# Kernel tuning notes

Measured on AMD Instinct MI355X. Metric: run time of the kernel, lower is better.

Reference implementation:

```python
import jax, jax.numpy as jnp
import numpy as np

D_HEAD = 64      # per-head dim (init d_head)
WINDOW = 64      # sliding_window_size
ROPE_BASE = 10000.0


def _rope(x):
    # x: [B, H, L, d] ; standard half-split rotary embedding over positions 0..L-1
    L, d = x.shape[-2], x.shape[-1]
    half = d // 2
    inv_freq = 1.0 / (ROPE_BASE ** (jnp.arange(half, dtype=jnp.float32) / half))
    ang = jnp.arange(L, dtype=jnp.float32)[:, None] * inv_freq  # [L, half]
    cos, sin = jnp.cos(ang), jnp.sin(ang)
    x1, x2 = x[..., :half], x[..., half:]
    return jnp.concatenate([x1 * cos - x2 * sin, x1 * sin + x2 * cos], axis=-1)


def setup_inputs() -> dict:
    key = jax.random.key(0)
    ks = jax.random.split(key, 4)
    B, L, D, H = 4, 2048, 2048, 2048
    nh = H // D_HEAD
    S = 16  # num_sinks
    u = jax.random.normal(ks[0], (B, L, D), jnp.float32)
    Wqkv = jax.random.normal(ks[1], (3 * H, D), jnp.float32) / np.sqrt(D)
    bqkv = jnp.zeros((3 * H,), jnp.float32)
    Wo = jax.random.normal(ks[2], (D, H), jnp.float32) / np.sqrt(H)
    bo = jnp.zeros((D,), jnp.float32)
    sinks = jax.random.normal(ks[3], (nh, S, D_HEAD), jnp.float32) / np.sqrt(D_HEAD)
    return {"u": u, "Wqkv": Wqkv, "bqkv": bqkv, "Wo": Wo, "bo": bo, "sinks": sinks}


def reference(u, Wqkv, bqkv, Wo, bo, sinks):
    B, L, D = u.shape
    d, w = D_HEAD, WINDOW
    nh, S, _ = sinks.shape
    scale = 1.0 / np.sqrt(d)

    qkv = u @ Wqkv.T + bqkv                         # [B, L, 3H]
    q, k, v = jnp.split(qkv, 3, axis=-1)
    heads = lambda x: x.reshape(B, L, nh, d).transpose(0, 2, 1, 3)  # [B, nh, L, d]
    q, k, v = heads(q), heads(k), heads(v)
    q, k = _rope(q), _rope(k)

    # Banded (sliding-window) attention in blocks of size w: query block i
    # attends key blocks {i-1, i, i+1} plus S global sink tokens.
    # Sink queries (prepended in the original) are discarded by O[:, :, -L:],
    # so we only compute attention for the L real queries.
    nb = L // w
    Qb = q.reshape(B, nh, nb, w, d)
    Kb = k.reshape(B, nh, nb, w, d)
    Vb = v.reshape(B, nh, nb, w, d)

    blk = jnp.arange(nb)[:, None] + jnp.arange(-1, 2)[None, :]   # [nb, 3]
    valid = (blk >= 0) & (blk < nb)
    blkc = jnp.clip(blk, 0, nb - 1)
    Kband = Kb[:, :, blkc].reshape(B, nh, nb, 3 * w, d)
    Vband = Vb[:, :, blkc].reshape(B, nh, nb, 3 * w, d)

    qpos = (jnp.arange(nb) * w)[:, None] + jnp.arange(w)          # [nb, w]
    kpos = ((blkc * w)[..., None] + jnp.arange(w)).reshape(nb, 3 * w)
    vmask = jnp.broadcast_to(valid[:, :, None], (nb, 3, w)).reshape(nb, 3 * w)
    mask = vmask[:, None, :] & (jnp.abs(qpos[:, :, None] - kpos[:, None, :]) <= w)  # [nb, w, 3w]

    s_band = jnp.einsum('bhnqd,bhnkd->bhnqk', Qb, Kband) * scale
    s_band = jnp.where(mask, s_band, -jnp.inf)
    s_sink = jnp.einsum('bhnqd,hsd->bhnqs', Qb, sinks) * scale    # sink K = sink param (no RoPE)
    p = jax.nn.softmax(jnp.concatenate([s_sink, s_band], axis=-1), axis=-1)

    O = (jnp.einsum('bhnqs,hsd->bhnqd', p[..., :S], sinks)        # sink V = sink param
         + jnp.einsum('bhnqk,bhnkd->bhnqd', p[..., S:], Vband))
    y = O.reshape(B, nh, L, d).transpose(0, 2, 1, 3).reshape(B, L, nh * d)
    return y @ Wo.T + bo
```

## Files before the change

### kernel.cpp

```cpp
#include <hip/hip_runtime.h>
#include <hip/hip_bf16.h>

typedef unsigned short u16;
typedef __attribute__((ext_vector_type(8))) short bf16x8;
typedef __attribute__((ext_vector_type(4))) float f32x4;

__device__ __forceinline__ u16 f2b(float f) {
  union { __hip_bfloat16 h; u16 u; } cv;
  cv.h = __float2bfloat16(f);
  return cv.u;
}
__device__ __forceinline__ float b2f(u16 u) {
  union { unsigned int i; float f; } cv;
  cv.i = ((unsigned int)u) << 16;
  return cv.f;
}

__global__ void cvt_bf16(const float* __restrict__ in, u16* __restrict__ out) {
  size_t i = ((size_t)blockIdx.x * 256 + threadIdx.x) * 4;
  float4 v = *(const float4*)(in + i);
  ushort4 o;
  o.x = f2b(v.x); o.y = f2b(v.y); o.z = f2b(v.z); o.w = f2b(v.w);
  *(ushort4*)(out + i) = o;
}

__global__ void rope_tab_k(float2* __restrict__ tab) {
  int t = blockIdx.x * 256 + threadIdx.x;
  int l = t >> 5, i = t & 31;
  float inv = powf(10000.0f, -(float)i * (1.0f / 32.0f));
  float ang = (float)l * inv;
  tab[t] = make_float2(cosf(ang), sinf(ang));
}

__global__ void rope_apply_k(u16* __restrict__ qkv, const float2* __restrict__ tab) {
  int idx = blockIdx.x * 256 + threadIdx.x;
  int i = idx & 31, h = (idx >> 5) & 31, row = idx >> 10;
  int l = row & 2047;
  float2 cs = tab[(l << 5) + i];
  size_t base = (size_t)row * 6144 + h * 64;
  #pragma unroll
  for (int t = 0; t < 2; ++t) {
    float x1 = b2f(qkv[base + i]);
    float x2 = b2f(qkv[base + 32 + i]);
    qkv[base + i]      = f2b(x1 * cs.x - x2 * cs.y);
    qkv[base + 32 + i] = f2b(x1 * cs.y + x2 * cs.x);
    base += 2048;
  }
}

template<bool BF16OUT>
__global__ __launch_bounds__(256) void gemm_bt(const u16* __restrict__ A,
                                               const u16* __restrict__ Bm,
                                               const float* __restrict__ bias,
                                               u16* __restrict__ Cb,
                                               float* __restrict__ Cf,
                                               int Ncols) {
  __shared__ u16 As[128 * 32];
  __shared__ u16 Bs[128 * 32];
  const int tid = threadIdx.x;
  const int lane = tid & 63, wid = tid >> 6;
  const int wr = wid >> 1, wc = wid & 1;
  const int m0 = blockIdx.y * 128, n0 = blockIdx.x * 128;
  const int lrow = lane >> 2;
  const int lcb  = (lane & 3) * 16;
  const int fr = lane & 15;
  const int fkb = (lane >> 4) * 16;
  f32x4 acc[4][4] = {};
  for (int k0 = 0; k0 < 2048; k0 += 32) {
    #pragma unroll
    for (int j = 0; j < 2; ++j) {
      int chunk = wid * 2 + j;
      int row = chunk * 16 + lrow;
      const char* ga = (const char*)(A + (size_t)(m0 + row) * 2048 + k0) + lcb;
      const char* gb = (const char*)(Bm + (size_t)(n0 + row) * 2048 + k0) + lcb;
      __builtin_amdgcn_global_load_lds((const __attribute__((address_space(1))) unsigned int*)ga,
                                       (__attribute__((address_space(3))) unsigned int*)(As + chunk * 512),
                                       16, 0, 0);
      __builtin_amdgcn_global_load_lds((const __attribute__((address_space(1))) unsigned int*)gb,
                                       (__attribute__((address_space(3))) unsigned int*)(Bs + chunk * 512),
                                       16, 0, 0);
    }
    __syncthreads();
    bf16x8 af[4], bfr[4];
    #pragma unroll
    for (int m = 0; m < 4; ++m)
      af[m] = *(const bf16x8*)((const char*)As + (wr * 64 + m * 16 + fr) * 64 + fkb);
    #pragma unroll
    for (int n = 0; n < 4; ++n)
      bfr[n] = *(const bf16x8*)((const char*)Bs + (wc * 64 + n * 16 + fr) * 64 + fkb);
    #pragma unroll
    for (int m = 0; m < 4; ++m)
      #pragma unroll
      for (int n = 0; n < 4; ++n)
        acc[m][n] = __builtin_amdgcn_mfma_f32_16x16x32_bf16(af[m], bfr[n], acc[m][n], 0, 0, 0);
    __syncthreads();
  }
  #pragma unroll
  for (int m = 0; m < 4; ++m) {
    #pragma unroll
    for (int n = 0; n < 4; ++n) {
      int gcol = n0 + wc * 64 + n * 16 + fr;
      int grow0 = m0 + wr * 64 + m * 16 + (lane >> 4) * 4;
      float bv = bias[gcol];
      #pragma unroll
      for (int r = 0; r < 4; ++r) {
        float v = acc[m][n][r] + bv;
        if (BF16OUT) Cb[(size_t)(grow0 + r) * Ncols + gcol] = f2b(v);
        else         Cf[(size_t)(grow0 + r) * Ncols + gcol] = v;
      }
    }
  }
}

#define PSTR 232
__global__ __launch_bounds__(256) void attn_k(const u16* __restrict__ qkv,
                                              const float* __restrict__ sinks,
                                              u16* __restrict__ O) {
  __shared__ char smem[59392];
  char* Kraw = smem;
  char* Qraw = smem + 28672;
  u16* Ps = (u16*)smem;
  u16* Vt = (u16*)(smem + 29696);
  const int tid = threadIdx.x, lane = tid & 63, wid = tid >> 6;
  const int fr = lane & 15, fk = lane >> 4;
  const int bx = blockIdx.x;
  const int n = bx & 31, h = (bx >> 5) & 31, b = bx >> 10;
  const size_t qrow0 = (size_t)b * 2048 + n * 64;

  for (int c = tid; c < 512; c += 256) {
    int row = c >> 3, colb = (c & 7) * 16;
    uint4 v = *(const uint4*)((const char*)(qkv + (qrow0 + row) * 6144 + h * 64) + colb);
    *(uint4*)(Qraw + ((row * 128 + colb) ^ ((row & 7) << 4))) = v;
  }
  {
    int row = tid >> 4, col4 = (tid & 15) * 4;
    float4 v = *(const float4*)(sinks + ((size_t)h * 16 + row) * 64 + col4);
    ushort4 o; o.x = f2b(v.x); o.y = f2b(v.y); o.z = f2b(v.z); o.w = f2b(v.w);
    *(ushort4*)(Kraw + ((row * 128 + col4 * 2) ^ ((row & 7) << 4))) = o;
  }
  for (int c = tid; c < 1536; c += 256) {
    int kidx = c >> 3, colb = (c & 7) * 16;
    int blk = n - 1 + (kidx >> 6);
    int blkc = min(max(blk, 0), 31);
    int kpos = blkc * 64 + (kidx & 63);
    uint4 v = *(const uint4*)((const char*)(qkv + ((size_t)b * 2048 + kpos) * 6144 + 2048 + h * 64) + colb);
    int row = 16 + kidx;
    *(uint4*)(Kraw + ((row * 128 + colb) ^ ((row & 7) << 4))) = v;
  }
  if (tid < 128) {
    int row = 208 + (tid >> 3), colb = (tid & 7) * 16;
    uint4 z = {0, 0, 0, 0};
    *(uint4*)(Kraw + ((row * 128 + colb) ^ ((row & 7) << 4))) = z;
  }
  __syncthreads();

  bf16x8 qf[2];
  {
    int qrow = wid * 16 + fr;
    #pragma unroll
    for (int kc = 0; kc < 2; ++kc)
      qf[kc] = *(const bf16x8*)(Qraw + ((qrow * 128 + kc * 64 + fk * 16) ^ ((qrow & 7) << 4)));
  }
  f32x4 sacc[14];
  #pragma unroll
  for (int g = 0; g < 14; ++g) {
    int key = g * 16 + fr;
    bf16x8 kf0 = *(const bf16x8*)(Kraw + ((key * 128 + fk * 16) ^ ((key & 7) << 4)));
    bf16x8 kf1 = *(const bf16x8*)(Kraw + ((key * 128 + 64 + fk * 16) ^ ((key & 7) << 4)));
    f32x4 a = {};
    a = __builtin_amdgcn_mfma_f32_16x16x32_bf16(qf[0], kf0, a, 0, 0, 0);
    a = __builtin_amdgcn_mfma_f32_16x16x32_bf16(qf[1], kf1, a, 0, 0, 0);
    sacc[g] = a;
  }
  float rowmax[4] = {-3e38f, -3e38f, -3e38f, -3e38f};
  #pragma unroll
  for (int g = 0; g < 14; ++g) {
    int key = g * 16 + fr;
    #pragma unroll
    for (int r = 0; r < 4; ++r) {
      float s = sacc[g][r] * 0.125f;
      bool valid;
      if (key < 16) valid = true;
      else if (key < 208) {
        int kidx = key - 16;
        int blk = n - 1 + (kidx >> 6);
        int kpos = blk * 64 + (kidx & 63);
        int qpos = n * 64 + wid * 16 + fk * 4 + r;
        valid = (blk >= 0) && (blk < 32) && (qpos - kpos <= 64) && (kpos - qpos <= 64);
      } else valid = false;
      s = valid ? s : -1e30f;
      sacc[g][r] = s;
      rowmax[r] = fmaxf(rowmax[r], s);
    }
  }
  #pragma unroll
  for (int d = 1; d < 16; d <<= 1)
    #pragma unroll
    for (int r = 0; r < 4; ++r)
      rowmax[r] = fmaxf(rowmax[r], __shfl_xor(rowmax[r], d));
  float rowsum[4] = {0, 0, 0, 0};
  #pragma unroll
  for (int g = 0; g < 14; ++g)
    #pragma unroll
    for (int r = 0; r < 4; ++r) {
      float p = __expf(sacc[g][r] - rowmax[r]);
      sacc[g][r] = p;
      rowsum[r] += p;
    }
  #pragma unroll
  for (int d = 1; d < 16; d <<= 1)
    #pragma unroll
    for (int r = 0; r < 4; ++r)
      rowsum[r] += __shfl_xor(rowsum[r], d);
  __syncthreads();

  #pragma unroll
  for (int g = 0; g < 14; ++g)
    #pragma unroll
    for (int r = 0; r < 4; ++r)
      Ps[(wid * 16 + fk * 4 + r) * PSTR + g * 16 + fr] = f2b(sacc[g][r]);
  {
    int dout = tid & 63, kb = tid >> 6;
    #pragma unroll
    for (int key = kb; key < 16; key += 4)
      Vt[dout * PSTR + key] = f2b(sinks[((size_t)h * 16 + key) * 64 + dout]);
    for (int kidx = kb; kidx < 192; kidx += 4) {
      int blk = n - 1 + (kidx >> 6);
      int blkc = min(max(blk, 0), 31);
      int kpos = blkc * 64 + (kidx & 63);
      Vt[dout * PSTR + 16 + kidx] = qkv[((size_t)b * 2048 + kpos) * 6144 + 4096 + h * 64 + dout];
    }
    #pragma unroll
    for (int key = 208 + kb; key < 224; key += 4)
      Vt[dout * PSTR + key] = 0;
  }
  __syncthreads();

  f32x4 oacc[4] = {};
  #pragma unroll
  for (int kc = 0; kc < 7; ++kc) {
    bf16x8 pf = *(const bf16x8*)(Ps + (wid * 16 + fr) * PSTR + kc * 32 + fk * 8);
    #pragma unroll
    for (int gd = 0; gd < 4; ++gd) {
      bf16x8 vf = *(const bf16x8*)(Vt + (gd * 16 + fr) * PSTR + kc * 32 + fk * 8);
      oacc[gd] = __builtin_amdgcn_mfma_f32_16x16x32_bf16(pf, vf, oacc[gd], 0, 0, 0);
    }
  }
  #pragma unroll
  for (int gd = 0; gd < 4; ++gd)
    #pragma unroll
    for (int r = 0; r < 4; ++r) {
      int qrl = wid * 16 + fk * 4 + r;
      float v = oacc[gd][r] / rowsum[r];
      O[(qrow0 + qrl) * 2048 + h * 64 + gd * 16 + fr] = f2b(v);
    }
}

extern "C" void kernel_launch(void* const* d_in, const int* in_sizes, int n_in,
                              void* d_out, int out_size, void* d_ws, size_t ws_size,
                              hipStream_t stream) {
  const float* u     = (const float*)d_in[0];
  const float* Wqkv  = (const float*)d_in[1];
  const float* bqkv  = (const float*)d_in[2];
  const float* Wo    = (const float*)d_in[3];
  const float* bo    = (const float*)d_in[4];
  const float* sinks = (const float*)d_in[5];
  float* out = (float*)d_out;

  char* ws = (char*)d_ws;
  u16* u_bf   = (u16*)ws;
  u16* w1_bf  = (u16*)(ws + 33554432);
  u16* qkv_bf = (u16*)(ws + 58720256);
  float2* tab = (float2*)(ws + 159383552);
  u16* O_bf  = u_bf;
  u16* w2_bf = w1_bf;

  cvt_bf16<<<16384, 256, 0, stream>>>(u, u_bf);
  cvt_bf16<<<12288, 256, 0, stream>>>(Wqkv, w1_bf);
  rope_tab_k<<<256, 256, 0, stream>>>(tab);
  gemm_bt<true><<<dim3(48, 64), 256, 0, stream>>>(u_bf, w1_bf, bqkv, qkv_bf, nullptr, 6144);
  rope_apply_k<<<32768, 256, 0, stream>>>(qkv_bf, tab);
  attn_k<<<4096, 256, 0, stream>>>(qkv_bf, sinks, O_bf);
  cvt_bf16<<<4096, 256, 0, stream>>>(Wo, w2_bf);
  gemm_bt<false><<<dim3(16, 64), 256, 0, stream>>>(O_bf, w2_bf, bo, nullptr, out, 2048);
}
```

Measured before the change: 624.5 us.

## Replace GEMM with 256x256 multi-stage pipelined kernel and fuse RoPE into epilogue

Swaps the simple single-buffered 128x128 GEMM for a 256x256-tile, 512-thread kernel. It uses a 4-slot LDS ring with three stages of global-to-LDS prefetch, explicit vmcnt waits, an XOR-swizzled LDS layout to reduce bank conflicts, and setprio around the MFMA block. The RoPE rotation is folded into the QKV GEMM epilogue by pairing accumulator columns n and n^2, which removes the separate read-modify-write pass over qkv. In exchange it needs 128KB of dynamic LDS per block. The output GEMM launches only 256 blocks, which may underfill the GPU.

```diff
diff --git a/kernel.cpp b/kernel.cpp
--- a/kernel.cpp
+++ b/kernel.cpp
@@ -32,81 +32,107 @@
   tab[t] = make_float2(cosf(ang), sinf(ang));
 }
 
-__global__ void rope_apply_k(u16* __restrict__ qkv, const float2* __restrict__ tab) {
-  int idx = blockIdx.x * 256 + threadIdx.x;
-  int i = idx & 31, h = (idx >> 5) & 31, row = idx >> 10;
-  int l = row & 2047;
-  float2 cs = tab[(l << 5) + i];
-  size_t base = (size_t)row * 6144 + h * 64;
-  #pragma unroll
-  for (int t = 0; t < 2; ++t) {
-    float x1 = b2f(qkv[base + i]);
-    float x2 = b2f(qkv[base + 32 + i]);
-    qkv[base + i]      = f2b(x1 * cs.x - x2 * cs.y);
-    qkv[base + 32 + i] = f2b(x1 * cs.y + x2 * cs.x);
-    base += 2048;
-  }
-}
-
-template<bool BF16OUT>
-__global__ __launch_bounds__(256) void gemm_bt(const u16* __restrict__ A,
-                                               const u16* __restrict__ Bm,
-                                               const float* __restrict__ bias,
-                                               u16* __restrict__ Cb,
-                                               float* __restrict__ Cf,
-                                               int Ncols) {
-  __shared__ u16 As[128 * 32];
-  __shared__ u16 Bs[128 * 32];
-  const int tid = threadIdx.x;
-  const int lane = tid & 63, wid = tid >> 6;
-  const int wr = wid >> 1, wc = wid & 1;
-  const int m0 = blockIdx.y * 128, n0 = blockIdx.x * 128;
-  const int lrow = lane >> 2;
-  const int lcb  = (lane & 3) * 16;
-  const int fr = lane & 15;
-  const int fkb = (lane >> 4) * 16;
-  f32x4 acc[4][4] = {};
-  for (int k0 = 0; k0 < 2048; k0 += 32) {
-    #pragma unroll
-    for (int j = 0; j < 2; ++j) {
-      int chunk = wid * 2 + j;
-      int row = chunk * 16 + lrow;
-      const char* ga = (const char*)(A + (size_t)(m0 + row) * 2048 + k0) + lcb;
-      const char* gb = (const char*)(Bm + (size_t)(n0 + row) * 2048 + k0) + lcb;
-      __builtin_amdgcn_global_load_lds((const __attribute__((address_space(1))) unsigned int*)ga,
-                                       (__attribute__((address_space(3))) unsigned int*)(As + chunk * 512),
-                                       16, 0, 0);
-      __builtin_amdgcn_global_load_lds((const __attribute__((address_space(1))) unsigned int*)gb,
-                                       (__attribute__((address_space(3))) unsigned int*)(Bs + chunk * 512),
-                                       16, 0, 0);
-    }
-    __syncthreads();
-    bf16x8 af[4], bfr[4];
-    #pragma unroll
-    for (int m = 0; m < 4; ++m)
-      af[m] = *(const bf16x8*)((const char*)As + (wr * 64 + m * 16 + fr) * 64 + fkb);
+template<int NCOLS, bool ROPE>
+__global__ __launch_bounds__(512, 2) void gemm_p(const u16* __restrict__ A,
+                                                 const u16* __restrict__ Bm,
+                                                 const float* __restrict__ bias,
+                                                 u16* __restrict__ Cb,
+                                                 float* __restrict__ Cf,
+                                                 const float2* __restrict__ tab) {
+  extern __shared__ char smem[];
+  u16* Asl = (u16*)smem;
+  u16* Bsl = (u16*)(smem + 65536);
+  const int tid = threadIdx.x, lane = tid & 63, w = tid >> 6;
+  const int wr = w >> 2, wcn = w & 3;
+  const int fr = lane & 15, fk = lane >> 4;
+  const int m0 = blockIdx.y * 256, n0 = blockIdx.x * 256;
+  const int srow = lane >> 2;
+  const int gslot = (lane & 3) ^ ((lane >> 3) & 3);
+  const int c0 = w * 2, c1 = c0 + 1;
+  const int sel = (fr >> 1) & 3;
+  const int ka = (fk ^ sel) << 4;
+  f32x4 acc[8][4] = {};
+
+  auto stage = [&](int jj) {
+    int slot = jj & 3;
+    int kk = jj * 32 + gslot * 8;
+    u16* Ad = Asl + slot * 8192;
+    u16* Bd = Bsl + slot * 8192;
+    const u16* gA0 = A  + (size_t)(m0 + c0 * 16 + srow) * 2048 + kk;
+    const u16* gA1 = A  + (size_t)(m0 + c1 * 16 + srow) * 2048 + kk;
+    const u16* gB0 = Bm + (size_t)(n0 + c0 * 16 + srow) * 2048 + kk;
+    const u16* gB1 = Bm + (size_t)(n0 + c1 * 16 + srow) * 2048 + kk;
+    __builtin_amdgcn_global_load_lds((const __attribute__((address_space(1))) unsigned int*)gA0,
+        (__attribute__((address_space(3))) unsigned int*)(Ad + c0 * 512), 16, 0, 0);
+    __builtin_amdgcn_global_load_lds((const __attribute__((address_space(1))) unsigned int*)gA1,
+        (__attribute__((address_space(3))) unsigned int*)(Ad + c1 * 512), 16, 0, 0);
+    __builtin_amdgcn_global_load_lds((const __attribute__((address_space(1))) unsigned int*)gB0,
+        (__attribute__((address_space(3))) unsigned int*)(Bd + c0 * 512), 16, 0, 0);
+    __builtin_amdgcn_global_load_lds((const __attribute__((address_space(1))) unsigned int*)gB1,
+        (__attribute__((address_space(3))) unsigned int*)(Bd + c1 * 512), 16, 0, 0);
+  };
+
+  stage(0); stage(1); stage(2);
+  asm volatile("s_waitcnt vmcnt(8)" ::: "memory");
+  asm volatile("s_barrier" ::: "memory");
+
+  for (int j = 0; j < 64; ++j) {
+    if (j < 61) stage(j + 3);
+    const char* Ab = (const char*)(Asl + (j & 3) * 8192);
+    const char* Bb = (const char*)(Bsl + (j & 3) * 8192);
+    bf16x8 af[8], bv[4];
+    #pragma unroll
+    for (int m = 0; m < 8; ++m)
+      af[m] = *(const bf16x8*)(Ab + (wr * 128 + m * 16 + fr) * 64 + ka);
     #pragma unroll
     for (int n = 0; n < 4; ++n)
-      bfr[n] = *(const bf16x8*)((const char*)Bs + (wc * 64 + n * 16 + fr) * 64 + fkb);
-    #pragma unroll
-    for (int m = 0; m < 4; ++m)
+      bv[n] = *(const bf16x8*)(Bb + (wcn * 64 + n * 16 + fr) * 64 + ka);
+    __builtin_amdgcn_s_setprio(1);
+    #pragma unroll
+    for (int m = 0; m < 8; ++m)
       #pragma unroll
       for (int n = 0; n < 4; ++n)
-        acc[m][n] = __builtin_amdgcn_mfma_f32_16x16x32_bf16(af[m], bfr[n], acc[m][n], 0, 0, 0);
-    __syncthreads();
-  }
-  #pragma unroll
-  for (int m = 0; m < 4; ++m) {
+        acc[m][n] = __builtin_amdgcn_mfma_f32_16x16x32_bf16(af[m], bv[n], acc[m][n], 0, 0, 0);
+    __builtin_amdgcn_s_setprio(0);
+    if (j < 61)       asm volatile("s_waitcnt vmcnt(8)" ::: "memory");
+    else if (j == 61) asm volatile("s_waitcnt vmcnt(4)" ::: "memory");
+    else if (j == 62) asm volatile("s_waitcnt vmcnt(0)" ::: "memory");
+    asm volatile("s_waitcnt lgkmcnt(0)" ::: "memory");
+    asm volatile("s_barrier" ::: "memory");
+  }
+
+  #pragma unroll
+  for (int m = 0; m < 8; ++m) {
+    int grow0 = m0 + wr * 128 + m * 16 + fk * 4;
     #pragma unroll
     for (int n = 0; n < 4; ++n) {
-      int gcol = n0 + wc * 64 + n * 16 + fr;
-      int grow0 = m0 + wr * 64 + m * 16 + (lane >> 4) * 4;
-      float bv = bias[gcol];
-      #pragma unroll
-      for (int r = 0; r < 4; ++r) {
-        float v = acc[m][n][r] + bv;
-        if (BF16OUT) Cb[(size_t)(grow0 + r) * Ncols + gcol] = f2b(v);
-        else         Cf[(size_t)(grow0 + r) * Ncols + gcol] = v;
+      int gcol = n0 + wcn * 64 + n * 16 + fr;
+      if (ROPE) {
+        if (gcol < 4096) {
+          int c = gcol & 63;
+          int i = c & 31;
+          bool lo = c < 32;
+          float bx = bias[gcol], bp = bias[gcol ^ 32];
+          #pragma unroll
+          for (int r = 0; r < 4; ++r) {
+            int t = grow0 + r;
+            float2 cs = tab[((t & 2047) << 5) + i];
+            float xb = acc[m][n][r] + bx;
+            float pb = acc[m][n ^ 2][r] + bp;
+            float o = lo ? (xb * cs.x - pb * cs.y) : (pb * cs.y + xb * cs.x);
+            Cb[(size_t)t * NCOLS + gcol] = f2b(o);
+          }
+        } else {
+          float bx = bias[gcol];
+          #pragma unroll
+          for (int r = 0; r < 4; ++r)
+            Cb[(size_t)(grow0 + r) * NCOLS + gcol] = f2b(acc[m][n][r] + bx);
+        }
+      } else {
+        float bx = bias[gcol];
+        #pragma unroll
+        for (int r = 0; r < 4; ++r)
+          Cf[(size_t)(grow0 + r) * NCOLS + gcol] = acc[m][n][r] + bx;
       }
     }
   }
@@ -275,12 +301,16 @@
   u16* O_bf  = u_bf;
   u16* w2_bf = w1_bf;
 
+  hipFuncSetAttribute((const void*)gemm_p<6144, true>,
+                      hipFuncAttributeMaxDynamicSharedMemorySize, 131072);
+  hipFuncSetAttribute((const void*)gemm_p<2048, false>,
+                      hipFuncAttributeMaxDynamicSharedMemorySize, 131072);
+
   cvt_bf16<<<16384, 256, 0, stream>>>(u, u_bf);
   cvt_bf16<<<12288, 256, 0, stream>>>(Wqkv, w1_bf);
   rope_tab_k<<<256, 256, 0, stream>>>(tab);
-  gemm_bt<true><<<dim3(48, 64), 256, 0, stream>>>(u_bf, w1_bf, bqkv, qkv_bf, nullptr, 6144);
-  rope_apply_k<<<32768, 256, 0, stream>>>(qkv_bf, tab);
+  gemm_p<6144, true><<<dim3(24, 32), 512, 131072, stream>>>(u_bf, w1_bf, bqkv, qkv_bf, nullptr, tab);
   attn_k<<<4096, 256, 0, stream>>>(qkv_bf, sinks, O_bf);
   cvt_bf16<<<4096, 256, 0, stream>>>(Wo, w2_bf);
-  gemm_bt<false><<<dim3(16, 64), 256, 0, stream>>>(O_bf, w2_bf, bo, nullptr, out, 2048);
-}
+  gemm_p<2048, false><<<dim3(8, 32), 512, 131072, stream>>>(O_bf, w2_bf, bo, nullptr, out, nullptr);
+}
```

Result: faster. 556.4 us (-10.9%).
